# Kernel tuning notes

Hardware: AMD Instinct MI355X
Metric: run time of the kernel (lower is better)

The kernel has to match this reference:

```python
import jax, jax.numpy as jnp
import numpy as np

BN_EPS = 1e-5


def setup_inputs() -> dict:
    key = jax.random.key(0)
    k = jax.random.split(key, 4)
    B, T, D, H, L = 32, 512, 1024, 1024, 3
    x = jax.random.normal(k[0], (B, T, D), dtype=jnp.float32)
    # Linear weights stored torch-style: out_features x in_features
    W = jax.random.normal(k[1], (L, 2 * H, D), dtype=jnp.float32) * 0.02
    U = jax.random.normal(k[2], (L, 2 * H, H), dtype=jnp.float32) * 0.02
    gamma = jnp.ones((L, 2 * H), dtype=jnp.float32)
    beta = jnp.zeros((L, 2 * H), dtype=jnp.float32)
    run_mean = jax.random.normal(k[3], (L, 2 * H), dtype=jnp.float32) * 0.01
    run_var = jnp.ones((L, 2 * H), dtype=jnp.float32)
    return dict(x=x, W=W, U=U, gamma=gamma, beta=beta,
                run_mean=run_mean, run_var=run_var)


def _ligru_layer(x, W, U, g, b, m, v):
    # x: [B,T,D]; W: [2H,D]; U: [2H,H]
    H = U.shape[1]
    w = jnp.einsum('btd,ed->bte', x, W)            # input projection, [B,T,2H]
    # BatchNorm1d in eval mode: per-channel affine with running stats
    w = (w - m) * (g * jax.lax.rsqrt(v + BN_EPS)) + b

    def step(h, wt):
        gates = wt + h @ U.T                        # [B,2H]
        at, zt = gates[:, :H], gates[:, H:]
        z = jax.nn.sigmoid(zt)
        hcand = jax.nn.relu(at)                     # drop_mask = 1 (eval)
        h = z * h + (1.0 - z) * hcand
        return h, h

    h0 = jnp.zeros((x.shape[0], H), dtype=x.dtype)  # h_init buffer
    _, hs = jax.lax.scan(step, h0, jnp.swapaxes(w, 0, 1))  # [T,B,H]
    return jnp.swapaxes(hs, 0, 1)                   # [B,T,H]


def reference(x, W, U, gamma, beta, run_mean, run_var):
    h_last = []
    for i in range(W.shape[0]):                     # loop over L=3 layers
        x = _ligru_layer(x, W[i], U[i], gamma[i], beta[i],
                         run_mean[i], run_var[i])
        h_last.append(x[:, -1])
    hh = jnp.stack(h_last, axis=1)                  # [B,L,H]
    return x, hh
```

## Files before the change

kernel.cpp:

```cpp
#include <hip/hip_runtime.h>
#include <hip/hip_bf16.h>
#include <stdint.h>

typedef _Float16 f16;
typedef _Float16 f16x8 __attribute__((ext_vector_type(8)));
typedef float f32x4 __attribute__((ext_vector_type(4)));

#define LDF16X8(p) (*reinterpret_cast<const f16x8*>(p))

__global__ __launch_bounds__(256) void k_cvt(const float* __restrict__ in,
                                             f16* __restrict__ out, int n) {
  int i = (blockIdx.x * 256 + threadIdx.x) * 4;
  if (i + 3 < n) {
    float4 v = *reinterpret_cast<const float4*>(in + i);
    out[i + 0] = (f16)v.x; out[i + 1] = (f16)v.y;
    out[i + 2] = (f16)v.z; out[i + 3] = (f16)v.w;
  } else {
    for (; i < n; ++i) out[i] = (f16)in[i];
  }
}

__global__ __launch_bounds__(256) void k_gemm_bn(
    const f16* __restrict__ A,
    const f16* __restrict__ B,
    const float* __restrict__ gamma, const float* __restrict__ beta,
    const float* __restrict__ mean, const float* __restrict__ var,
    f16* __restrict__ out,
    int M, int N, int K) {
  __shared__ f16 Al[4 * 128 * 8];
  __shared__ f16 Bl[4 * 128 * 8];
  const int tid = threadIdx.x;
  const int lane = tid & 63, wid = tid >> 6;
  const int wm = wid >> 1, wn = wid & 1;
  const int row0 = blockIdx.x * 128, col0 = blockIdx.y * 128;

  f32x4 acc[4][4] = {};

  const int sR = tid >> 1;
  const int sk8 = (tid & 1) * 2;

  for (int k0 = 0; k0 < K; k0 += 32) {
    __syncthreads();
    {
      const f16* srcA = A + (size_t)(row0 + sR) * K + k0 + sk8 * 8;
      uint4 a0 = *reinterpret_cast<const uint4*>(srcA);
      uint4 a1 = *reinterpret_cast<const uint4*>(srcA + 8);
      *reinterpret_cast<uint4*>(&Al[(sk8 * 128 + sR) * 8]) = a0;
      *reinterpret_cast<uint4*>(&Al[((sk8 + 1) * 128 + sR) * 8]) = a1;
      const f16* srcB = B + (size_t)(col0 + sR) * K + k0 + sk8 * 8;
      uint4 b0 = *reinterpret_cast<const uint4*>(srcB);
      uint4 b1 = *reinterpret_cast<const uint4*>(srcB + 8);
      *reinterpret_cast<uint4*>(&Bl[(sk8 * 128 + sR) * 8]) = b0;
      *reinterpret_cast<uint4*>(&Bl[((sk8 + 1) * 128 + sR) * 8]) = b1;
    }
    __syncthreads();

    const int k8 = lane >> 4, r16 = lane & 15;
    f16x8 af[4], bfr[4];
#pragma unroll
    for (int m = 0; m < 4; ++m)
      af[m] = LDF16X8(&Al[(k8 * 128 + wm * 64 + m * 16 + r16) * 8]);
#pragma unroll
    for (int n = 0; n < 4; ++n)
      bfr[n] = LDF16X8(&Bl[(k8 * 128 + wn * 64 + n * 16 + r16) * 8]);
#pragma unroll
    for (int m = 0; m < 4; ++m)
#pragma unroll
      for (int n = 0; n < 4; ++n)
        acc[m][n] = __builtin_amdgcn_mfma_f32_16x16x32_f16(af[m], bfr[n], acc[m][n], 0, 0, 0);
  }

#pragma unroll
  for (int n = 0; n < 4; ++n) {
    int col = col0 + wn * 64 + n * 16 + (lane & 15);
    float g = gamma[col], be = beta[col], mu = mean[col], va = var[col];
    float s = g * rsqrtf(va + 1e-5f);
    float sh = be - mu * s;
#pragma unroll
    for (int m = 0; m < 4; ++m) {
#pragma unroll
      for (int r = 0; r < 4; ++r) {
        int row = row0 + wm * 64 + m * 16 + (lane >> 4) * 4 + r;
        out[(size_t)row * N + col] = (f16)(acc[m][n][r] * s + sh);
      }
    }
  }
}

__global__ __launch_bounds__(256) void k_scan(
    const float* __restrict__ U,
    const f16* __restrict__ w,
    f16* __restrict__ hpub,
    f16* __restrict__ xoutH,
    float* __restrict__ xoutF,
    float* __restrict__ hh,
    unsigned* __restrict__ flags,
    int layer, int last, int nwg) {
  __shared__ f16 Ul[16 * 1024];
  __shared__ float gl[2][32][16];

  const int tid = threadIdx.x;
  const int lane = tid & 63, wid = tid >> 6;
  const int mt = wid & 1, kh = wid >> 1;
  const int j0 = blockIdx.x * 8;

  for (int i = tid; i < 16 * 1024; i += 256) {
    int e = i >> 10, k = i & 1023;
    int erow = (e < 8) ? (j0 + e) : (1024 + j0 + e - 8);
    Ul[((k >> 3) * 16 + e) * 8 + (k & 7)] = (f16)U[(size_t)erow * 1024 + k];
  }
  __syncthreads();

  const int cb = tid >> 3;
  const int cj = tid & 7;
  float hreg = 0.f;

  const int r16 = lane & 15, kg4 = lane >> 4;

  float wa = (float)w[(size_t)(cb * 512) * 2048 + j0 + cj];
  float wz = (float)w[(size_t)(cb * 512) * 2048 + 1024 + j0 + cj];

  for (int t = 0; t < 512; ++t) {
    const int cur = t & 1, nxt = cur ^ 1;

    f32x4 acc = {};
    const f16* hbase = hpub + cur * 32768 + (size_t)(mt * 16 + r16) * 1024 + kh * 512 + kg4 * 8;
#pragma unroll
    for (int kk = 0; kk < 16; ++kk) {
      f16x8 a = LDF16X8(hbase + kk * 32);
      f16x8 b = LDF16X8(&Ul[((kh * 64 + kk * 4 + kg4) * 16 + r16) * 8]);
      acc = __builtin_amdgcn_mfma_f32_16x16x32_f16(a, b, acc, 0, 0, 0);
    }
#pragma unroll
    for (int r = 0; r < 4; ++r)
      gl[kh][mt * 16 + kg4 * 4 + r][r16] = acc[r];
    __syncthreads();

    {
      float apre = gl[0][cb][cj] + gl[1][cb][cj] + wa;
      float zpre = gl[0][cb][8 + cj] + gl[1][cb][8 + cj] + wz;
      float z = 1.f / (1.f + expf(-zpre));
      float hn = z * hreg + (1.f - z) * fmaxf(apre, 0.f);
      hreg = hn;
      hpub[nxt * 32768 + cb * 1024 + j0 + cj] = (f16)hn;
      size_t xoff = (size_t)(cb * 512 + t) * 1024 + j0 + cj;
      if (last) xoutF[xoff] = hn;
      else      xoutH[xoff] = (f16)hn;
      if (t == 511) hh[(size_t)(cb * 3 + layer) * 1024 + j0 + cj] = hn;
    }

    if (t + 1 < 512) {
      size_t wrow = (size_t)(cb * 512 + t + 1) * 2048;
      wa = (float)w[wrow + j0 + cj];
      wz = (float)w[wrow + 1024 + j0 + cj];
    }

    __syncthreads();
    if (tid == 0) {
      __builtin_amdgcn_fence(__ATOMIC_RELEASE, "agent");
      __hip_atomic_store(&flags[(size_t)blockIdx.x * 32], (unsigned)(t + 1),
                         __ATOMIC_RELAXED, __HIP_MEMORY_SCOPE_AGENT);
    }
    if (tid < 64) {
      while (__hip_atomic_load(&flags[(size_t)tid * 32], __ATOMIC_RELAXED,
                               __HIP_MEMORY_SCOPE_AGENT) < (unsigned)(t + 1))
        __builtin_amdgcn_s_sleep(1);
      while (__hip_atomic_load(&flags[(size_t)(64 + tid) * 32], __ATOMIC_RELAXED,
                               __HIP_MEMORY_SCOPE_AGENT) < (unsigned)(t + 1))
        __builtin_amdgcn_s_sleep(1);
      __builtin_amdgcn_fence(__ATOMIC_ACQUIRE, "agent");
    }
    __syncthreads();
  }
}

extern "C" void kernel_launch(void* const* d_in, const int* in_sizes, int n_in,
                              void* d_out, int out_size, void* d_ws, size_t ws_size,
                              hipStream_t stream) {
  const float* x     = (const float*)d_in[0];
  const float* W     = (const float*)d_in[1];
  const float* U     = (const float*)d_in[2];
  const float* gamma = (const float*)d_in[3];
  const float* beta  = (const float*)d_in[4];
  const float* rmean = (const float*)d_in[5];
  const float* rvar  = (const float*)d_in[6];
  float* outX  = (float*)d_out;
  float* outHH = outX + (size_t)32 * 512 * 1024;

  f16* xb = (f16*)d_out;

  char* ws = (char*)d_ws;
  f16* wbuf = (f16*)(ws);
  f16* Wb   = (f16*)(ws + 67108864);
  f16* hpub = (f16*)(ws + 71303168);
  unsigned* flags = (unsigned*)(ws + 71434240);

  k_cvt<<<16384, 256, 0, stream>>>(x, xb, 16777216);

  for (int l = 0; l < 3; ++l) {
    k_cvt<<<2048, 256, 0, stream>>>(W + (size_t)l * 2097152, Wb, 2097152);
    k_gemm_bn<<<dim3(128, 16), 256, 0, stream>>>(
        xb, Wb, gamma + l * 2048, beta + l * 2048, rmean + l * 2048, rvar + l * 2048,
        wbuf, 16384, 2048, 1024);
    hipMemsetAsync(hpub, 0, 131072, stream);
    hipMemsetAsync(flags, 0, 16384, stream);
    k_scan<<<128, 256, 0, stream>>>(
        U + (size_t)l * 2097152, wbuf, hpub,
        xb, outX, outHH, flags, l, (l == 2) ? 1 : 0, 128);
  }
}
```

Baseline: 10.20 ms.

## Replace release/acquire fences with relaxed atomic h publication in recurrent scan

The per-step grid barrier in the recurrent scan drops the agent-scope release and acquire fences. Instead, the hidden state is published with relaxed agent-scope atomic stores and read back with relaxed atomic 64-bit loads, so coherence no longer depends on cache flushes. Pairs of f16 values are packed with a lane shuffle so each store is 32 bits. The two flag polls are merged into one loop, and the final hh write is moved out of the loop. Correctness now relies on relaxed atomics plus store ordering instead of explicit fences, which is a memory-model risk.

```diff
diff --git a/kernel.cpp b/kernel.cpp
--- a/kernel.cpp
+++ b/kernel.cpp
@@ -5,8 +5,16 @@
 typedef _Float16 f16;
 typedef _Float16 f16x8 __attribute__((ext_vector_type(8)));
 typedef float f32x4 __attribute__((ext_vector_type(4)));
+typedef unsigned long long u64;
 
 #define LDF16X8(p) (*reinterpret_cast<const f16x8*>(p))
+
+__device__ __forceinline__ f16x8 ld_h(const f16* p) {
+  union { u64 q[2]; f16x8 v; } u;
+  u.q[0] = __hip_atomic_load((const u64*)p,     __ATOMIC_RELAXED, __HIP_MEMORY_SCOPE_AGENT);
+  u.q[1] = __hip_atomic_load((const u64*)p + 1, __ATOMIC_RELAXED, __HIP_MEMORY_SCOPE_AGENT);
+  return u.v;
+}
 
 __global__ __launch_bounds__(256) void k_cvt(const float* __restrict__ in,
                                              f16* __restrict__ out, int n) {
@@ -127,7 +135,7 @@
     const f16* hbase = hpub + cur * 32768 + (size_t)(mt * 16 + r16) * 1024 + kh * 512 + kg4 * 8;
 #pragma unroll
     for (int kk = 0; kk < 16; ++kk) {
-      f16x8 a = LDF16X8(hbase + kk * 32);
+      f16x8 a = ld_h(hbase + kk * 32);
       f16x8 b = LDF16X8(&Ul[((kh * 64 + kk * 4 + kg4) * 16 + r16) * 8]);
       acc = __builtin_amdgcn_mfma_f32_16x16x32_f16(a, b, acc, 0, 0, 0);
     }
@@ -142,11 +150,15 @@
       float z = 1.f / (1.f + expf(-zpre));
       float hn = z * hreg + (1.f - z) * fmaxf(apre, 0.f);
       hreg = hn;
-      hpub[nxt * 32768 + cb * 1024 + j0 + cj] = (f16)hn;
+      f16 hf = (f16)hn;
+      unsigned hb = (unsigned)__builtin_bit_cast(unsigned short, hf);
+      unsigned nb = __shfl_down(hb, 1, 64);
+      if ((cj & 1) == 0)
+        __hip_atomic_store((unsigned*)(hpub + nxt * 32768 + cb * 1024 + j0 + cj),
+                           hb | (nb << 16), __ATOMIC_RELAXED, __HIP_MEMORY_SCOPE_AGENT);
       size_t xoff = (size_t)(cb * 512 + t) * 1024 + j0 + cj;
       if (last) xoutF[xoff] = hn;
       else      xoutH[xoff] = (f16)hn;
-      if (t == 511) hh[(size_t)(cb * 3 + layer) * 1024 + j0 + cj] = hn;
     }
 
     if (t + 1 < 512) {
@@ -156,22 +168,24 @@
     }
 
     __syncthreads();
-    if (tid == 0) {
-      __builtin_amdgcn_fence(__ATOMIC_RELEASE, "agent");
-      __hip_atomic_store(&flags[(size_t)blockIdx.x * 32], (unsigned)(t + 1),
+    if (tid == 0)
+      __hip_atomic_store(&flags[(size_t)blockIdx.x * 32], t + 1u,
                          __ATOMIC_RELAXED, __HIP_MEMORY_SCOPE_AGENT);
-    }
     if (tid < 64) {
-      while (__hip_atomic_load(&flags[(size_t)tid * 32], __ATOMIC_RELAXED,
-                               __HIP_MEMORY_SCOPE_AGENT) < (unsigned)(t + 1))
+      const unsigned tgt = t + 1u;
+      for (;;) {
+        unsigned a = __hip_atomic_load(&flags[(size_t)tid * 32],
+                                       __ATOMIC_RELAXED, __HIP_MEMORY_SCOPE_AGENT);
+        unsigned b = __hip_atomic_load(&flags[(size_t)(64 + tid) * 32],
+                                       __ATOMIC_RELAXED, __HIP_MEMORY_SCOPE_AGENT);
+        if (a >= tgt && b >= tgt) break;
         __builtin_amdgcn_s_sleep(1);
-      while (__hip_atomic_load(&flags[(size_t)(64 + tid) * 32], __ATOMIC_RELAXED,
-                               __HIP_MEMORY_SCOPE_AGENT) < (unsigned)(t + 1))
-        __builtin_amdgcn_s_sleep(1);
-      __builtin_amdgcn_fence(__ATOMIC_ACQUIRE, "agent");
-    }
-    __syncthreads();
-  }
+      }
+    }
+    __syncthreads();
+  }
+
+  hh[(size_t)(cb * 3 + layer) * 1024 + j0 + cj] = hreg;
 }
 
 extern "C" void kernel_launch(void* const* d_in, const int* in_sizes, int n_in,
```

After: 9.618 ms. 5.7% less time.
